# Performance work log

Measured on AMD Instinct MI355X. Metric: run time of the kernel, lower is better.

## Reference

```python
import jax, jax.numpy as jnp
import numpy as np

# ---- static synthetic forest: 64 complete binary trees, depth 9 (heap layout) ----
DEPTH = 9
N_TREES = 64
C = 8
M = 256
N_GEN = 8
NPT = 2 ** (DEPTH + 1) - 1          # 1023 nodes per tree
DIM = N_TREES * NPT                  # 65472 total nodes
_base = np.arange(N_TREES) * NPT

def _lvl_nodes(l):
    return (_base[:, None] + np.arange(2 ** l - 1, 2 ** (l + 1) - 1)[None, :]).reshape(-1)

LEVELS = []   # list of (parent_idx, child_idx) edge arrays, top level first
UPAR = []     # unique parents per level (== nodes of level l-1)
for _l in range(1, DEPTH + 1):
    _ch = np.arange(2 ** _l - 1, 2 ** (_l + 1) - 1)
    _pa = (_ch - 1) // 2
    LEVELS.append((jnp.asarray((_base[:, None] + _pa[None, :]).reshape(-1)),
                   jnp.asarray((_base[:, None] + _ch[None, :]).reshape(-1))))
    UPAR.append(jnp.asarray(_lvl_nodes(_l - 1)))
LEAVES = jnp.asarray(_lvl_nodes(DEPTH))
ROOTS = jnp.asarray(_base)
INTERNAL = jnp.asarray(np.concatenate([_lvl_nodes(l) for l in range(DEPTH)]))
TREES_IND = jnp.asarray(np.repeat(np.arange(N_TREES), NPT))
N_CH = 2.0  # every internal node has exactly 2 children -> segment mean = sum/2


def _forward(A, B, Pi, x):
    # softmax reparameterization (per generative head)
    sm_A = jax.nn.softmax(A, axis=0)          # (C,C,G), softmax over parent-state dim 0
    sm_B = jax.nn.softmax(B, axis=1)          # (C,M,G), softmax over symbols
    sm_Pi = jax.nn.softmax(Pi, axis=0)        # (C,G)

    # B[:, x] gathered per node, as (node, C, G)
    B_x = jnp.transpose(sm_B[:, x], (1, 0, 2))  # (DIM,C,G)

    # ---- reversed upward (leaves -> roots) ----
    beta = jnp.zeros((DIM, C, N_GEN), dtype=A.dtype)
    t_beta = jnp.zeros((DIM, C, N_GEN), dtype=A.dtype)
    b_leaf = sm_Pi[None, :, :] * B_x[LEAVES]                 # (L,C,G)
    beta = beta.at[LEAVES].set(b_leaf / b_leaf.sum(1, keepdims=True))
    for (pa, ch), upar in zip(reversed(LEVELS), reversed(UPAR)):
        beta_ch = beta[ch]                                   # (E,C,G)
        t_beta_ch = jnp.einsum('ijg,ejg->eig', sm_A, beta_ch)
        t_beta = t_beta + jax.ops.segment_sum(t_beta_ch, pa, num_segments=DIM) / N_CH
        beta_l = t_beta[upar] * B_x[upar]                    # (U,C,G)
        beta = beta.at[upar].set(beta_l / beta_l.sum(1, keepdims=True))

    # ---- reversed downward (roots -> leaves) ----
    eps = jnp.zeros((DIM, C, N_GEN), dtype=A.dtype)
    t_eps = jnp.zeros((DIM, C, C, N_GEN), dtype=A.dtype)
    eps = eps.at[ROOTS].set(beta[ROOTS])
    for pa, ch in LEVELS:
        # (E,Cpa,Cch,G)
        eps_joint = (eps[pa][:, :, None, :] * sm_A[None]
                     * beta[ch][:, None, :, :] / t_beta[pa][:, :, None, :])
        t_eps = t_eps + jax.ops.segment_sum(eps_joint, pa, num_segments=DIM) / N_CH
        eps = eps.at[ch].set(eps_joint.sum(1))

    # ---- log-likelihood ----
    lik = jnp.zeros((DIM, N_GEN), dtype=A.dtype)
    lik = lik.at[INTERNAL].add((t_eps[INTERNAL] * jnp.log(sm_A)[None]).sum((1, 2)))
    lik = lik + (eps * jnp.log(B_x)).sum(1)  # all_nodes == all nodes here
    lik = lik.at[LEAVES].add((eps[LEAVES] * jnp.log(sm_Pi)[None]).sum(1))
    ll = jax.ops.segment_sum(lik, TREES_IND, num_segments=N_TREES)  # (n_trees,G)
    return -ll


def setup_inputs() -> dict:
    key = jax.random.key(0)
    k1, k2, k3, k4 = jax.random.split(key, 4)
    A = jax.random.uniform(k1, (C, C, N_GEN), minval=-5.0, maxval=5.0)
    B = jax.random.uniform(k2, (C, M, N_GEN), minval=-5.0, maxval=5.0)
    Pi = jax.random.uniform(k3, (C, N_GEN), minval=-5.0, maxval=5.0)
    x = jax.random.randint(k4, (DIM,), 0, M)
    return {"A": A, "B": B, "Pi": Pi, "x": x}


def reference(A, B, Pi, x):
    return _forward(A, B, Pi, x)
```

## Files before the change

### kernel.cpp

```cpp
#include <hip/hip_runtime.h>

#define NT 256

namespace {
constexpr int C = 8, G = 8, M = 256, NPT = 1023, NINT = 511;

__global__ __launch_bounds__(NT, 2)
void htmm_fused(const float* __restrict__ Ag, const float* __restrict__ Bg,
                const float* __restrict__ Pig, const int* __restrict__ xg,
                float* __restrict__ out)
{
    __shared__ int   xs[NPT + 1];
    __shared__ float smB[C][M + 1];
    __shared__ float logB[C][M + 1];
    __shared__ float beta[NPT][9];
    __shared__ float tbe[NINT][9];
    __shared__ float smA_s[C][9];
    __shared__ float alA_s[C][9];
    __shared__ float pi_s[2][C];
    __shared__ float red[4];

    const int tid  = threadIdx.x;
    const int wv   = tid >> 6;
    const int lane = tid & 63;
    const int s    = lane >> 3;
    const int q    = lane & 7;
    const int tree = blockIdx.x >> 3, g = blockIdx.x & 7;

    for (int n = tid; n < NPT; n += NT) xs[n] = xg[tree * NPT + n];

    {
        const int i  = 2 * wv + (lane >> 5);
        const int c0 = lane & 31;
        float raw[8], ex[8], ssum = 0.f;
        #pragma unroll
        for (int t = 0; t < 8; ++t) {
            raw[t] = Bg[(i * M + c0 + 32 * t) * G + g];
            ex[t]  = __expf(raw[t]);
            ssum  += ex[t];
        }
        #pragma unroll
        for (int m = 1; m <= 16; m <<= 1) ssum += __shfl_xor(ssum, m);
        const float inv = 1.f / ssum, ls = __logf(ssum);
        #pragma unroll
        for (int t = 0; t < 8; ++t) {
            smB[i][c0 + 32 * t]  = ex[t] * inv;
            logB[i][c0 + 32 * t] = raw[t] - ls;
        }
    }
    if (wv == 0) {
        const float raw = Ag[(s * C + q) * G + g];
        float e = __expf(raw), S = e;
        #pragma unroll
        for (int m = 8; m <= 32; m <<= 1) S += __shfl_xor(S, m);
        const float v = e / S;
        smA_s[s][q] = v;
        alA_s[s][q] = v * (raw - __logf(S));
    } else if (wv == 1 && lane < C) {
        const float raw = Pig[lane * G + g];
        float e = __expf(raw), S = e;
        #pragma unroll
        for (int m = 1; m <= 4; m <<= 1) S += __shfl_xor(S, m);
        pi_s[0][lane] = e / S;
        pi_s[1][lane] = raw - __logf(S);
    }
    __syncthreads();

    float Arow[8], Acol[8], ALc[8], piR[8];
    #pragma unroll
    for (int j = 0; j < 8; ++j) Arow[j] = smA_s[q][j];
    #pragma unroll
    for (int i = 0; i < 8; ++i) { Acol[i] = smA_s[i][q]; ALc[i] = alA_s[i][q]; piR[i] = pi_s[0][i]; }
    const float logPi_q = pi_s[1][q];

    float acc = 0.f;

    auto upstep = [&](int p) {
        const int cl = 2 * p + 1;
        float tb = 0.f;
        #pragma unroll
        for (int j = 0; j < 8; ++j) tb += Arow[j] * (beta[cl][j] + beta[cl + 1][j]);
        tb *= 0.5f;
        tbe[p][q] = tb;
        float u = tb * smB[q][xs[p]];
        float S = u;
        #pragma unroll
        for (int m = 1; m <= 4; m <<= 1) S += __shfl_xor(S, m);
        beta[p][q] = u / S;
    };
    auto wstep = [&](int p) {
        tbe[p][q] = beta[p][q] / tbe[p][q];
    };
    auto dstep = [&](int ch, int p, bool leaf) {
        float es = 0.f, ts = 0.f;
        #pragma unroll
        for (int i = 0; i < 8; ++i) {
            const float w = tbe[p][i];
            es += w * Acol[i];
            ts += w * ALc[i];
        }
        const float br = beta[ch][q];
        const float ev = br * es;
        acc += 0.5f * br * ts + ev * logB[q][xs[ch]];
        if (leaf) acc += ev * logPi_q;
        else      beta[ch][q] = ev;
    };

    #pragma unroll
    for (int g2 = 0; g2 < 2; ++g2) {
        const int k0 = 16 * wv + 8 * g2, k = k0 + s;
        {
            const int n  = 511 + 8 * k0 + lane;
            const int xv = xs[n];
            float u[8], S = 0.f;
            #pragma unroll
            for (int i = 0; i < 8; ++i) { u[i] = piR[i] * smB[i][xv]; S += u[i]; }
            const float inv = 1.f / S;
            #pragma unroll
            for (int i = 0; i < 8; ++i) beta[n][i] = u[i] * inv;
        }
        __builtin_amdgcn_wave_barrier();
        #pragma unroll
        for (int m = 0; m < 4; ++m) upstep(255 + 4 * k + m);
        __builtin_amdgcn_wave_barrier();
        #pragma unroll
        for (int m = 0; m < 2; ++m) upstep(127 + 2 * k + m);
        __builtin_amdgcn_wave_barrier();
        upstep(63 + k);
        __builtin_amdgcn_wave_barrier();
    }
    __syncthreads();

    if (wv == 0) {
        for (int d = 5; d >= 0; --d) {
            const int Pd = 1 << d, base = Pd - 1;
            for (int r0 = 0; r0 < Pd; r0 += 8)
                if (r0 + s < Pd) upstep(base + r0 + s);
            __builtin_amdgcn_wave_barrier();
        }
        if (lane < 8) acc += beta[0][lane] * logB[lane][xs[0]];
        for (int dc = 1; dc <= 6; ++dc) {
            const int Pp = 1 << (dc - 1), basep = Pp - 1, basec = 2 * Pp - 1, NC = 2 * Pp;
            for (int r0 = 0; r0 < Pp; r0 += 8)
                if (r0 + s < Pp) wstep(basep + r0 + s);
            __builtin_amdgcn_wave_barrier();
            for (int r0 = 0; r0 < NC; r0 += 8)
                if (r0 + s < NC) {
                    const int cr = r0 + s;
                    dstep(basec + cr, basep + (cr >> 1), false);
                }
            __builtin_amdgcn_wave_barrier();
        }
    }
    __syncthreads();

    #pragma unroll
    for (int g2 = 0; g2 < 2; ++g2) {
        const int k = 16 * wv + 8 * g2 + s;
        wstep(63 + k);
        __builtin_amdgcn_wave_barrier();
        #pragma unroll
        for (int m = 0; m < 2; ++m) dstep(127 + 2 * k + m, 63 + k, false);
        __builtin_amdgcn_wave_barrier();
        #pragma unroll
        for (int m = 0; m < 2; ++m) wstep(127 + 2 * k + m);
        __builtin_amdgcn_wave_barrier();
        #pragma unroll
        for (int m = 0; m < 4; ++m) dstep(255 + 4 * k + m, 127 + 2 * k + (m >> 1), false);
        __builtin_amdgcn_wave_barrier();
        #pragma unroll
        for (int m = 0; m < 4; ++m) wstep(255 + 4 * k + m);
        __builtin_amdgcn_wave_barrier();
        #pragma unroll
        for (int m = 0; m < 8; ++m) dstep(511 + 8 * k + m, 255 + 4 * k + (m >> 1), true);
    }

    #pragma unroll
    for (int m = 1; m <= 32; m <<= 1) acc += __shfl_xor(acc, m);
    if (lane == 0) red[wv] = acc;
    __syncthreads();
    if (tid == 0) out[blockIdx.x] = -(red[0] + red[1] + red[2] + red[3]);
}
}

extern "C" void kernel_launch(void* const* d_in, const int* in_sizes, int n_in,
                              void* d_out, int out_size, void* d_ws, size_t ws_size,
                              hipStream_t stream) {
    const float* A  = (const float*)d_in[0];
    const float* Bm = (const float*)d_in[1];
    const float* Pi = (const float*)d_in[2];
    const int*   x  = (const int*)d_in[3];
    float* o = (float*)d_out;
    hipLaunchKernelGGL(htmm_fused, dim3(64 * 8), dim3(NT), 0, stream,
                       A, Bm, Pi, x, o);
}
```

Measured before the change: 76.02 us.

## Keep bottom tree levels in registers and exchange via lane shuffles

The bottom three levels of each tree (leaves through level 6 subtree roots) now stay in per-lane registers for both the upward and downward passes. Child state vectors move between lanes with width-8 shuffles instead of round-trips through shared memory, and the shared beta/tbe arrays shrink to the top 127/63 nodes. Divisions are also replaced with the hardware reciprocal. This removes LDS traffic and intra-wave barriers but raises register pressure, which could hurt occupancy under launch_bounds(256,2), and the reciprocal is slightly less precise.

Result: no change. 74.89 us (-1.5%).

```diff
diff --git a/kernel.cpp b/kernel.cpp
--- a/kernel.cpp
+++ b/kernel.cpp
@@ -3,7 +3,9 @@
 #define NT 256
 
 namespace {
-constexpr int C = 8, G = 8, M = 256, NPT = 1023, NINT = 511;
+constexpr int C = 8, G = 8, M = 256, NPT = 1023;
+
+__device__ __forceinline__ float rcpf(float x) { return __builtin_amdgcn_rcpf(x); }
 
 __global__ __launch_bounds__(NT, 2)
 void htmm_fused(const float* __restrict__ Ag, const float* __restrict__ Bg,
@@ -13,8 +15,8 @@
     __shared__ int   xs[NPT + 1];
     __shared__ float smB[C][M + 1];
     __shared__ float logB[C][M + 1];
-    __shared__ float beta[NPT][9];
-    __shared__ float tbe[NINT][9];
+    __shared__ float beta_t[127][9];
+    __shared__ float tbe_t[63][9];
     __shared__ float smA_s[C][9];
     __shared__ float alA_s[C][9];
     __shared__ float pi_s[2][C];
@@ -41,7 +43,7 @@
         }
         #pragma unroll
         for (int m = 1; m <= 16; m <<= 1) ssum += __shfl_xor(ssum, m);
-        const float inv = 1.f / ssum, ls = __logf(ssum);
+        const float inv = rcpf(ssum), ls = __logf(ssum);
         #pragma unroll
         for (int t = 0; t < 8; ++t) {
             smB[i][c0 + 32 * t]  = ex[t] * inv;
@@ -66,68 +68,61 @@
     }
     __syncthreads();
 
-    float Arow[8], Acol[8], ALc[8], piR[8];
+    float Arow[8], Acol[8], ALc[8];
     #pragma unroll
     for (int j = 0; j < 8; ++j) Arow[j] = smA_s[q][j];
     #pragma unroll
-    for (int i = 0; i < 8; ++i) { Acol[i] = smA_s[i][q]; ALc[i] = alA_s[i][q]; piR[i] = pi_s[0][i]; }
-    const float logPi_q = pi_s[1][q];
+    for (int i = 0; i < 8; ++i) { Acol[i] = smA_s[i][q]; ALc[i] = alA_s[i][q]; }
+    const float pi_q = pi_s[0][q], logPi_q = pi_s[1][q];
 
     float acc = 0.f;
 
-    auto upstep = [&](int p) {
-        const int cl = 2 * p + 1;
-        float tb = 0.f;
-        #pragma unroll
-        for (int j = 0; j < 8; ++j) tb += Arow[j] * (beta[cl][j] + beta[cl + 1][j]);
-        tb *= 0.5f;
-        tbe[p][q] = tb;
-        float u = tb * smB[q][xs[p]];
-        float S = u;
-        #pragma unroll
-        for (int m = 1; m <= 4; m <<= 1) S += __shfl_xor(S, m);
-        beta[p][q] = u / S;
-    };
-    auto wstep = [&](int p) {
-        tbe[p][q] = beta[p][q] / tbe[p][q];
-    };
-    auto dstep = [&](int ch, int p, bool leaf) {
-        float es = 0.f, ts = 0.f;
-        #pragma unroll
-        for (int i = 0; i < 8; ++i) {
-            const float w = tbe[p][i];
-            es += w * Acol[i];
-            ts += w * ALc[i];
-        }
-        const float br = beta[ch][q];
-        const float ev = br * es;
-        acc += 0.5f * br * ts + ev * logB[q][xs[ch]];
-        if (leaf) acc += ev * logPi_q;
-        else      beta[ch][q] = ev;
-    };
-
-    #pragma unroll
-    for (int g2 = 0; g2 < 2; ++g2) {
-        const int k0 = 16 * wv + 8 * g2, k = k0 + s;
+    float b9[2][8], tb8[2][4], b8[2][4], tb7[2][2], b7[2][2], tb6[2];
+    #pragma unroll
+    for (int h = 0; h < 2; ++h) {
+        const int k = 16 * wv + 8 * h + s;
+        #pragma unroll
+        for (int m = 0; m < 8; ++m) {
+            float u = pi_q * smB[q][xs[511 + 8 * k + m]];
+            float S = u;
+            S += __shfl_xor(S, 1); S += __shfl_xor(S, 2); S += __shfl_xor(S, 4);
+            b9[h][m] = u * rcpf(S);
+        }
+        #pragma unroll
+        for (int m = 0; m < 4; ++m) {
+            float c = b9[h][2 * m] + b9[h][2 * m + 1];
+            float tb = 0.f;
+            #pragma unroll
+            for (int j = 0; j < 8; ++j) tb += Arow[j] * __shfl(c, j, 8);
+            tb *= 0.5f; tb8[h][m] = tb;
+            float u = tb * smB[q][xs[255 + 4 * k + m]];
+            float S = u;
+            S += __shfl_xor(S, 1); S += __shfl_xor(S, 2); S += __shfl_xor(S, 4);
+            b8[h][m] = u * rcpf(S);
+        }
+        #pragma unroll
+        for (int m = 0; m < 2; ++m) {
+            float c = b8[h][2 * m] + b8[h][2 * m + 1];
+            float tb = 0.f;
+            #pragma unroll
+            for (int j = 0; j < 8; ++j) tb += Arow[j] * __shfl(c, j, 8);
+            tb *= 0.5f; tb7[h][m] = tb;
+            float u = tb * smB[q][xs[127 + 2 * k + m]];
+            float S = u;
+            S += __shfl_xor(S, 1); S += __shfl_xor(S, 2); S += __shfl_xor(S, 4);
+            b7[h][m] = u * rcpf(S);
+        }
         {
-            const int n  = 511 + 8 * k0 + lane;
-            const int xv = xs[n];
-            float u[8], S = 0.f;
-            #pragma unroll
-            for (int i = 0; i < 8; ++i) { u[i] = piR[i] * smB[i][xv]; S += u[i]; }
-            const float inv = 1.f / S;
-            #pragma unroll
-            for (int i = 0; i < 8; ++i) beta[n][i] = u[i] * inv;
-        }
-        __builtin_amdgcn_wave_barrier();
-        #pragma unroll
-        for (int m = 0; m < 4; ++m) upstep(255 + 4 * k + m);
-        __builtin_amdgcn_wave_barrier();
-        #pragma unroll
-        for (int m = 0; m < 2; ++m) upstep(127 + 2 * k + m);
-        __builtin_amdgcn_wave_barrier();
-        upstep(63 + k);
-        __builtin_amdgcn_wave_barrier();
+            float c = b7[h][0] + b7[h][1];
+            float tb = 0.f;
+            #pragma unroll
+            for (int j = 0; j < 8; ++j) tb += Arow[j] * __shfl(c, j, 8);
+            tb *= 0.5f; tb6[h] = tb;
+            float u = tb * smB[q][xs[63 + k]];
+            float S = u;
+            S += __shfl_xor(S, 1); S += __shfl_xor(S, 2); S += __shfl_xor(S, 4);
+            beta_t[63 + k][q] = u * rcpf(S);
+        }
     }
     __syncthreads();
 
@@ -135,44 +130,92 @@
         for (int d = 5; d >= 0; --d) {
             const int Pd = 1 << d, base = Pd - 1;
             for (int r0 = 0; r0 < Pd; r0 += 8)
-                if (r0 + s < Pd) upstep(base + r0 + s);
-            __builtin_amdgcn_wave_barrier();
-        }
-        if (lane < 8) acc += beta[0][lane] * logB[lane][xs[0]];
-        for (int dc = 1; dc <= 6; ++dc) {
-            const int Pp = 1 << (dc - 1), basep = Pp - 1, basec = 2 * Pp - 1, NC = 2 * Pp;
-            for (int r0 = 0; r0 < Pp; r0 += 8)
-                if (r0 + s < Pp) wstep(basep + r0 + s);
-            __builtin_amdgcn_wave_barrier();
-            for (int r0 = 0; r0 < NC; r0 += 8)
-                if (r0 + s < NC) {
-                    const int cr = r0 + s;
-                    dstep(basec + cr, basep + (cr >> 1), false);
+                if (r0 + s < Pd) {
+                    const int p = base + r0 + s, cl = 2 * p + 1;
+                    float tb = 0.f;
+                    #pragma unroll
+                    for (int j = 0; j < 8; ++j) tb += Arow[j] * (beta_t[cl][j] + beta_t[cl + 1][j]);
+                    tb *= 0.5f; tbe_t[p][q] = tb;
+                    float u = tb * smB[q][xs[p]];
+                    float S = u;
+                    S += __shfl_xor(S, 1); S += __shfl_xor(S, 2); S += __shfl_xor(S, 4);
+                    beta_t[p][q] = u * rcpf(S);
                 }
             __builtin_amdgcn_wave_barrier();
         }
-    }
-    __syncthreads();
-
-    #pragma unroll
-    for (int g2 = 0; g2 < 2; ++g2) {
-        const int k = 16 * wv + 8 * g2 + s;
-        wstep(63 + k);
-        __builtin_amdgcn_wave_barrier();
-        #pragma unroll
-        for (int m = 0; m < 2; ++m) dstep(127 + 2 * k + m, 63 + k, false);
-        __builtin_amdgcn_wave_barrier();
-        #pragma unroll
-        for (int m = 0; m < 2; ++m) wstep(127 + 2 * k + m);
-        __builtin_amdgcn_wave_barrier();
-        #pragma unroll
-        for (int m = 0; m < 4; ++m) dstep(255 + 4 * k + m, 127 + 2 * k + (m >> 1), false);
-        __builtin_amdgcn_wave_barrier();
-        #pragma unroll
-        for (int m = 0; m < 4; ++m) wstep(255 + 4 * k + m);
-        __builtin_amdgcn_wave_barrier();
-        #pragma unroll
-        for (int m = 0; m < 8; ++m) dstep(511 + 8 * k + m, 255 + 4 * k + (m >> 1), true);
+        if (lane < 8) acc += beta_t[0][lane] * logB[lane][xs[0]];
+        for (int dc = 1; dc <= 6; ++dc) {
+            const int Pp = 1 << (dc - 1), basep = Pp - 1, basec = 2 * Pp - 1, NCc = 2 * Pp;
+            for (int r0 = 0; r0 < Pp; r0 += 8)
+                if (r0 + s < Pp) {
+                    const int p = basep + r0 + s;
+                    tbe_t[p][q] = beta_t[p][q] * rcpf(tbe_t[p][q]);
+                }
+            __builtin_amdgcn_wave_barrier();
+            for (int r0 = 0; r0 < NCc; r0 += 8)
+                if (r0 + s < NCc) {
+                    const int cr = r0 + s, ch = basec + cr, p = basep + (cr >> 1);
+                    float es = 0.f, ts = 0.f;
+                    #pragma unroll
+                    for (int i = 0; i < 8; ++i) {
+                        const float w = tbe_t[p][i];
+                        es += w * Acol[i]; ts += w * ALc[i];
+                    }
+                    const float br = beta_t[ch][q];
+                    const float ev = br * es;
+                    acc += 0.5f * br * ts + ev * logB[q][xs[ch]];
+                    beta_t[ch][q] = ev;
+                }
+            __builtin_amdgcn_wave_barrier();
+        }
+    }
+    __syncthreads();
+
+    #pragma unroll
+    for (int h = 0; h < 2; ++h) {
+        const int k = 16 * wv + 8 * h + s;
+        const float w6 = beta_t[63 + k][q] * rcpf(tb6[h]);
+        float w7[2], w8[4];
+        #pragma unroll
+        for (int m = 0; m < 2; ++m) {
+            float es = 0.f, ts = 0.f;
+            #pragma unroll
+            for (int i = 0; i < 8; ++i) {
+                const float wi = __shfl(w6, i, 8);
+                es += wi * Acol[i]; ts += wi * ALc[i];
+            }
+            const float br = b7[h][m];
+            const float ev = br * es;
+            acc += 0.5f * br * ts + ev * logB[q][xs[127 + 2 * k + m]];
+            w7[m] = ev * rcpf(tb7[h][m]);
+        }
+        #pragma unroll
+        for (int m = 0; m < 4; ++m) {
+            const float wp = w7[m >> 1];
+            float es = 0.f, ts = 0.f;
+            #pragma unroll
+            for (int i = 0; i < 8; ++i) {
+                const float wi = __shfl(wp, i, 8);
+                es += wi * Acol[i]; ts += wi * ALc[i];
+            }
+            const float br = b8[h][m];
+            const float ev = br * es;
+            acc += 0.5f * br * ts + ev * logB[q][xs[255 + 4 * k + m]];
+            w8[m] = ev * rcpf(tb8[h][m]);
+        }
+        #pragma unroll
+        for (int m = 0; m < 8; ++m) {
+            const float wp = w8[m >> 1];
+            float es = 0.f, ts = 0.f;
+            #pragma unroll
+            for (int i = 0; i < 8; ++i) {
+                const float wi = __shfl(wp, i, 8);
+                es += wi * Acol[i]; ts += wi * ALc[i];
+            }
+            const float br = b9[h][m];
+            const float ev = br * es;
+            acc += 0.5f * br * ts + ev * (logB[q][xs[511 + 8 * k + m]] + logPi_q);
+        }
     }
 
     #pragma unroll
```

## Remap tree passes to one thread per node with register-resident A and leaves

Applied to the files above, without the earlier changes.

Replaces the lane-per-state mapping (8 lanes per node, shuffles for normalization) with one thread per node holding the full 8-state vector. All of A and A*logA live in registers, and the transposed B tables are read with float4 loads. The bottom two levels (leaves and level 8) are kept in registers per thread, which shrinks shared memory and cuts traffic. The upper levels now run on very few active threads with a block-wide barrier per level, whereas before they ran on a single wave with wave barriers. The 128 extra registers for A may also reduce occupancy or cause spills.

Measured after the change: 90.02 us. 1.18x slower.

```diff
diff --git a/kernel.cpp b/kernel.cpp
--- a/kernel.cpp
+++ b/kernel.cpp
@@ -3,32 +3,41 @@
 #define NT 256
 
 namespace {
-constexpr int C = 8, G = 8, M = 256, NPT = 1023, NINT = 511;
+constexpr int C = 8, G = 8, M = 256, NPT = 1023;
+constexpr int PD = 12;
+
+__device__ __forceinline__ float rcpf(float x) { return __builtin_amdgcn_rcpf(x); }
+
+#define LD8(dst, srcp) do {                                              \
+    const float4 _a = *(const float4*)(srcp);                            \
+    const float4 _b = *(const float4*)((srcp) + 4);                      \
+    (dst)[0]=_a.x;(dst)[1]=_a.y;(dst)[2]=_a.z;(dst)[3]=_a.w;             \
+    (dst)[4]=_b.x;(dst)[5]=_b.y;(dst)[6]=_b.z;(dst)[7]=_b.w; } while(0)
+
+#define ST8(dstp, src) do {                                              \
+    *(float4*)(dstp)       = make_float4((src)[0],(src)[1],(src)[2],(src)[3]); \
+    *(float4*)((dstp) + 4) = make_float4((src)[4],(src)[5],(src)[6],(src)[7]); } while(0)
 
 __global__ __launch_bounds__(NT, 2)
 void htmm_fused(const float* __restrict__ Ag, const float* __restrict__ Bg,
                 const float* __restrict__ Pig, const int* __restrict__ xg,
                 float* __restrict__ out)
 {
-    __shared__ int   xs[NPT + 1];
-    __shared__ float smB[C][M + 1];
-    __shared__ float logB[C][M + 1];
-    __shared__ float beta[NPT][9];
-    __shared__ float tbe[NINT][9];
-    __shared__ float smA_s[C][9];
-    __shared__ float alA_s[C][9];
+    __shared__ int xs[NPT + 1];
+    __shared__ __align__(16) float smBt[M][PD];
+    __shared__ __align__(16) float logBt[M][PD];
+    __shared__ __align__(16) float bet[511][PD];
+    __shared__ __align__(16) float tbe[255][PD];
+    __shared__ __align__(16) float smA_s[C][C];
+    __shared__ __align__(16) float alA_s[C][C];
     __shared__ float pi_s[2][C];
     __shared__ float red[4];
 
     const int tid  = threadIdx.x;
-    const int wv   = tid >> 6;
-    const int lane = tid & 63;
-    const int s    = lane >> 3;
-    const int q    = lane & 7;
+    const int wv   = tid >> 6, lane = tid & 63;
     const int tree = blockIdx.x >> 3, g = blockIdx.x & 7;
 
     for (int n = tid; n < NPT; n += NT) xs[n] = xg[tree * NPT + n];
-
     {
         const int i  = 2 * wv + (lane >> 5);
         const int c0 = lane & 31;
@@ -41,21 +50,22 @@
         }
         #pragma unroll
         for (int m = 1; m <= 16; m <<= 1) ssum += __shfl_xor(ssum, m);
-        const float inv = 1.f / ssum, ls = __logf(ssum);
+        const float inv = rcpf(ssum), ls = __logf(ssum);
         #pragma unroll
         for (int t = 0; t < 8; ++t) {
-            smB[i][c0 + 32 * t]  = ex[t] * inv;
-            logB[i][c0 + 32 * t] = raw[t] - ls;
+            smBt [c0 + 32 * t][i] = ex[t] * inv;
+            logBt[c0 + 32 * t][i] = raw[t] - ls;
         }
     }
     if (wv == 0) {
-        const float raw = Ag[(s * C + q) * G + g];
+        const int si = lane >> 3, qj = lane & 7;
+        const float raw = Ag[(si * C + qj) * G + g];
         float e = __expf(raw), S = e;
         #pragma unroll
         for (int m = 8; m <= 32; m <<= 1) S += __shfl_xor(S, m);
         const float v = e / S;
-        smA_s[s][q] = v;
-        alA_s[s][q] = v * (raw - __logf(S));
+        smA_s[si][qj] = v;
+        alA_s[si][qj] = v * (raw - __logf(S));
     } else if (wv == 1 && lane < C) {
         const float raw = Pig[lane * G + g];
         float e = __expf(raw), S = e;
@@ -66,113 +76,190 @@
     }
     __syncthreads();
 
-    float Arow[8], Acol[8], ALc[8], piR[8];
+    float Ae[64], ALAe[64], piR[8], lPi[8];
     #pragma unroll
-    for (int j = 0; j < 8; ++j) Arow[j] = smA_s[q][j];
+    for (int i = 0; i < 8; ++i) {
+        float ar[8], lr[8];
+        LD8(ar, &smA_s[i][0]);
+        LD8(lr, &alA_s[i][0]);
+        #pragma unroll
+        for (int j = 0; j < 8; ++j) { Ae[8*i+j] = ar[j]; ALAe[8*i+j] = lr[j]; }
+    }
     #pragma unroll
-    for (int i = 0; i < 8; ++i) { Acol[i] = smA_s[i][q]; ALc[i] = alA_s[i][q]; piR[i] = pi_s[0][i]; }
-    const float logPi_q = pi_s[1][q];
+    for (int i = 0; i < 8; ++i) { piR[i] = pi_s[0][i]; lPi[i] = pi_s[1][i]; }
+
+    const int nd8 = 255 + tid;
+    const int xv8 = xs[nd8], xvL = xs[2*nd8 + 1], xvR = xs[2*nd8 + 2];
+    float bl0[8], bl1[8], tb8[8], b8[8];
+    {
+        float sm[8], u[8], S, inv;
+        LD8(sm, &smBt[xvL][0]);
+        S = 0.f;
+        #pragma unroll
+        for (int i = 0; i < 8; ++i) { u[i] = piR[i] * sm[i]; S += u[i]; }
+        inv = rcpf(S);
+        #pragma unroll
+        for (int i = 0; i < 8; ++i) bl0[i] = u[i] * inv;
+
+        LD8(sm, &smBt[xvR][0]);
+        S = 0.f;
+        #pragma unroll
+        for (int i = 0; i < 8; ++i) { u[i] = piR[i] * sm[i]; S += u[i]; }
+        inv = rcpf(S);
+        #pragma unroll
+        for (int i = 0; i < 8; ++i) bl1[i] = u[i] * inv;
+
+        float c[8];
+        #pragma unroll
+        for (int j = 0; j < 8; ++j) c[j] = bl0[j] + bl1[j];
+        #pragma unroll
+        for (int i = 0; i < 8; ++i) {
+            float t = 0.f;
+            #pragma unroll
+            for (int j = 0; j < 8; ++j) t += Ae[8*i+j] * c[j];
+            tb8[i] = 0.5f * t;
+        }
+        LD8(sm, &smBt[xv8][0]);
+        S = 0.f;
+        #pragma unroll
+        for (int i = 0; i < 8; ++i) { u[i] = tb8[i] * sm[i]; S += u[i]; }
+        inv = rcpf(S);
+        #pragma unroll
+        for (int i = 0; i < 8; ++i) b8[i] = u[i] * inv;
+        ST8(&bet[nd8][0], b8);
+    }
+    __syncthreads();
+
+    for (int lvl = 7; lvl >= 0; --lvl) {
+        const int cnt = 1 << lvl, base = cnt - 1;
+        if (tid < cnt) {
+            const int p = base + tid, cl = 2*p + 1;
+            float lb_[8], rb_[8], cb[8];
+            LD8(lb_, &bet[cl][0]);
+            LD8(rb_, &bet[cl + 1][0]);
+            #pragma unroll
+            for (int j = 0; j < 8; ++j) cb[j] = lb_[j] + rb_[j];
+            float tb[8];
+            #pragma unroll
+            for (int i = 0; i < 8; ++i) {
+                float t = 0.f;
+                #pragma unroll
+                for (int j = 0; j < 8; ++j) t += Ae[8*i+j] * cb[j];
+                tb[i] = 0.5f * t;
+            }
+            ST8(&tbe[p][0], tb);
+            float sm[8], u[8], S = 0.f;
+            LD8(sm, &smBt[xs[p]][0]);
+            #pragma unroll
+            for (int i = 0; i < 8; ++i) { u[i] = tb[i] * sm[i]; S += u[i]; }
+            const float inv = rcpf(S);
+            float b[8];
+            #pragma unroll
+            for (int i = 0; i < 8; ++i) b[i] = u[i] * inv;
+            ST8(&bet[p][0], b);
+        }
+        __syncthreads();
+    }
 
     float acc = 0.f;
-
-    auto upstep = [&](int p) {
-        const int cl = 2 * p + 1;
-        float tb = 0.f;
-        #pragma unroll
-        for (int j = 0; j < 8; ++j) tb += Arow[j] * (beta[cl][j] + beta[cl + 1][j]);
-        tb *= 0.5f;
-        tbe[p][q] = tb;
-        float u = tb * smB[q][xs[p]];
-        float S = u;
-        #pragma unroll
-        for (int m = 1; m <= 4; m <<= 1) S += __shfl_xor(S, m);
-        beta[p][q] = u / S;
-    };
-    auto wstep = [&](int p) {
-        tbe[p][q] = beta[p][q] / tbe[p][q];
-    };
-    auto dstep = [&](int ch, int p, bool leaf) {
-        float es = 0.f, ts = 0.f;
+    if (tid == 0) {
+        float b0[8], lb[8];
+        LD8(b0, &bet[0][0]);
+        LD8(lb, &logBt[xs[0]][0]);
+        #pragma unroll
+        for (int j = 0; j < 8; ++j) acc += b0[j] * lb[j];
+    }
+
+    for (int dc = 1; dc <= 7; ++dc) {
+        const int cnt = 1 << dc, base = cnt - 1;
+        if (tid < cnt) {
+            const int ch = base + tid, p = (ch - 1) >> 1;
+            float ep[8], tp[8], w[8];
+            LD8(ep, &bet[p][0]);
+            LD8(tp, &tbe[p][0]);
+            #pragma unroll
+            for (int i = 0; i < 8; ++i) w[i] = ep[i] * rcpf(tp[i]);
+            float es[8] = {0,0,0,0,0,0,0,0}, ts[8] = {0,0,0,0,0,0,0,0};
+            #pragma unroll
+            for (int i = 0; i < 8; ++i) {
+                #pragma unroll
+                for (int j = 0; j < 8; ++j) {
+                    es[j] += w[i] * Ae[8*i+j];
+                    ts[j] += w[i] * ALAe[8*i+j];
+                }
+            }
+            float bc[8], lb[8], ev[8];
+            LD8(bc, &bet[ch][0]);
+            LD8(lb, &logBt[xs[ch]][0]);
+            float a1 = 0.f, a2 = 0.f;
+            #pragma unroll
+            for (int j = 0; j < 8; ++j) {
+                ev[j] = bc[j] * es[j];
+                a1 += bc[j] * ts[j];
+                a2 += ev[j] * lb[j];
+            }
+            acc += 0.5f * a1 + a2;
+            ST8(&bet[ch][0], ev);
+        }
+        __syncthreads();
+    }
+
+    {
+        const int p7 = (nd8 - 1) >> 1;
+        float ep[8], tp[8], w[8];
+        LD8(ep, &bet[p7][0]);
+        LD8(tp, &tbe[p7][0]);
+        #pragma unroll
+        for (int i = 0; i < 8; ++i) w[i] = ep[i] * rcpf(tp[i]);
+        float es[8] = {0,0,0,0,0,0,0,0}, ts[8] = {0,0,0,0,0,0,0,0};
         #pragma unroll
         for (int i = 0; i < 8; ++i) {
-            const float w = tbe[p][i];
-            es += w * Acol[i];
-            ts += w * ALc[i];
-        }
-        const float br = beta[ch][q];
-        const float ev = br * es;
-        acc += 0.5f * br * ts + ev * logB[q][xs[ch]];
-        if (leaf) acc += ev * logPi_q;
-        else      beta[ch][q] = ev;
-    };
-
-    #pragma unroll
-    for (int g2 = 0; g2 < 2; ++g2) {
-        const int k0 = 16 * wv + 8 * g2, k = k0 + s;
-        {
-            const int n  = 511 + 8 * k0 + lane;
-            const int xv = xs[n];
-            float u[8], S = 0.f;
-            #pragma unroll
-            for (int i = 0; i < 8; ++i) { u[i] = piR[i] * smB[i][xv]; S += u[i]; }
-            const float inv = 1.f / S;
-            #pragma unroll
-            for (int i = 0; i < 8; ++i) beta[n][i] = u[i] * inv;
-        }
-        __builtin_amdgcn_wave_barrier();
-        #pragma unroll
-        for (int m = 0; m < 4; ++m) upstep(255 + 4 * k + m);
-        __builtin_amdgcn_wave_barrier();
-        #pragma unroll
-        for (int m = 0; m < 2; ++m) upstep(127 + 2 * k + m);
-        __builtin_amdgcn_wave_barrier();
-        upstep(63 + k);
-        __builtin_amdgcn_wave_barrier();
-    }
-    __syncthreads();
-
-    if (wv == 0) {
-        for (int d = 5; d >= 0; --d) {
-            const int Pd = 1 << d, base = Pd - 1;
-            for (int r0 = 0; r0 < Pd; r0 += 8)
-                if (r0 + s < Pd) upstep(base + r0 + s);
-            __builtin_amdgcn_wave_barrier();
-        }
-        if (lane < 8) acc += beta[0][lane] * logB[lane][xs[0]];
-        for (int dc = 1; dc <= 6; ++dc) {
-            const int Pp = 1 << (dc - 1), basep = Pp - 1, basec = 2 * Pp - 1, NC = 2 * Pp;
-            for (int r0 = 0; r0 < Pp; r0 += 8)
-                if (r0 + s < Pp) wstep(basep + r0 + s);
-            __builtin_amdgcn_wave_barrier();
-            for (int r0 = 0; r0 < NC; r0 += 8)
-                if (r0 + s < NC) {
-                    const int cr = r0 + s;
-                    dstep(basec + cr, basep + (cr >> 1), false);
-                }
-            __builtin_amdgcn_wave_barrier();
-        }
-    }
-    __syncthreads();
-
-    #pragma unroll
-    for (int g2 = 0; g2 < 2; ++g2) {
-        const int k = 16 * wv + 8 * g2 + s;
-        wstep(63 + k);
-        __builtin_amdgcn_wave_barrier();
-        #pragma unroll
-        for (int m = 0; m < 2; ++m) dstep(127 + 2 * k + m, 63 + k, false);
-        __builtin_amdgcn_wave_barrier();
-        #pragma unroll
-        for (int m = 0; m < 2; ++m) wstep(127 + 2 * k + m);
-        __builtin_amdgcn_wave_barrier();
-        #pragma unroll
-        for (int m = 0; m < 4; ++m) dstep(255 + 4 * k + m, 127 + 2 * k + (m >> 1), false);
-        __builtin_amdgcn_wave_barrier();
-        #pragma unroll
-        for (int m = 0; m < 4; ++m) wstep(255 + 4 * k + m);
-        __builtin_amdgcn_wave_barrier();
-        #pragma unroll
-        for (int m = 0; m < 8; ++m) dstep(511 + 8 * k + m, 255 + 4 * k + (m >> 1), true);
+            #pragma unroll
+            for (int j = 0; j < 8; ++j) {
+                es[j] += w[i] * Ae[8*i+j];
+                ts[j] += w[i] * ALAe[8*i+j];
+            }
+        }
+        float lb[8], ev8[8], w8[8];
+        LD8(lb, &logBt[xv8][0]);
+        float a1 = 0.f, a2 = 0.f;
+        #pragma unroll
+        for (int j = 0; j < 8; ++j) {
+            ev8[j] = b8[j] * es[j];
+            a1 += b8[j] * ts[j];
+            a2 += ev8[j] * lb[j];
+        }
+        acc += 0.5f * a1 + a2;
+        #pragma unroll
+        for (int i = 0; i < 8; ++i) w8[i] = ev8[i] * rcpf(tb8[i]);
+
+        float es2[8] = {0,0,0,0,0,0,0,0}, ts2[8] = {0,0,0,0,0,0,0,0};
+        #pragma unroll
+        for (int i = 0; i < 8; ++i) {
+            #pragma unroll
+            for (int j = 0; j < 8; ++j) {
+                es2[j] += w8[i] * Ae[8*i+j];
+                ts2[j] += w8[i] * ALAe[8*i+j];
+            }
+        }
+        LD8(lb, &logBt[xvL][0]);
+        a1 = 0.f; a2 = 0.f;
+        #pragma unroll
+        for (int j = 0; j < 8; ++j) {
+            const float ev = bl0[j] * es2[j];
+            a1 += bl0[j] * ts2[j];
+            a2 += ev * (lb[j] + lPi[j]);
+        }
+        acc += 0.5f * a1 + a2;
+        LD8(lb, &logBt[xvR][0]);
+        a1 = 0.f; a2 = 0.f;
+        #pragma unroll
+        for (int j = 0; j < 8; ++j) {
+            const float ev = bl1[j] * es2[j];
+            a1 += bl1[j] * ts2[j];
+            a2 += ev * (lb[j] + lPi[j]);
+        }
+        acc += 0.5f * a1 + a2;
     }
 
     #pragma unroll
```
